# Optimization experiments

Measured on AMD Instinct MI355X. Metric: run time of the kernel, lower is better.

Reference implementation:

```python
import jax, jax.numpy as jnp
import numpy as np

TEMP = 0.05          # args.temp_lp_loss
NUM_CLASSES = 256

def _l2norm(x):
    return x / jnp.linalg.norm(x, axis=-1, keepdims=True)

def setup_inputs() -> dict:
    key = jax.random.key(0)
    k1, k2, k3 = jax.random.split(key, 3)
    B, C, Bs, TOPK = 2048, 2048, 4096, 4
    feats = _l2norm(jax.random.normal(k1, (B, C), jnp.float32))
    feats_s = _l2norm(jax.random.normal(k2, (Bs, TOPK, C), jnp.float32))
    labels = jax.random.randint(k3, (B,), 0, NUM_CLASSES, dtype=jnp.int32)
    # every class 0..255 appears, so each query has >=1 positive support
    labels_s = jnp.arange(Bs * TOPK, dtype=jnp.int32) % NUM_CLASSES
    return {"feats": feats, "feats_s": feats_s, "labels": labels, "labels_s": labels_s}

def reference(feats, feats_s, labels, labels_s):
    Bs, topk, C = feats_s.shape
    fs = feats_s.reshape(Bs * topk, C)                    # [N, C]
    E = jnp.exp(jnp.einsum('bc,nc->bn', feats, fs) / TEMP)  # [B, N]
    is_pos = labels[:, None] == labels_s[None, :]          # [B, N]
    # per-row hardest positive (min over positives of exp-sim)
    pos_min = jnp.min(jnp.where(is_pos, E, jnp.inf), axis=1)   # [B]
    # sum over all negatives of exp-sim
    neg_sum = jnp.sum(jnp.where(is_pos, 0.0, E), axis=1)       # [B]
    loss = -jnp.log(pos_min / (pos_min + neg_sum + 1e-6) + 1e-6)
    return jnp.mean(loss)
```

## Files before the change

kernel.cpp:

```cpp
#include <hip/hip_runtime.h>
#include <hip/hip_bf16.h>
#include <stdint.h>

#define M_TOTAL 2048
#define N_TOTAL 16384
#define K_TOTAL 2048
#define NPARTS  256

#define SCALE_E8M0 0x76767676
#define SCALE_F 512.0f

typedef __attribute__((ext_vector_type(4))) int   int4v;
typedef __attribute__((ext_vector_type(8))) int   int8v;
typedef __attribute__((ext_vector_type(4))) float floatx4;

__global__ void cvt_fp8(const float4* __restrict__ src, uint32_t* __restrict__ dst, int n4) {
    int i = blockIdx.x * blockDim.x + threadIdx.x;
    const int stride = gridDim.x * blockDim.x;
    for (; i < n4; i += stride) {
        float4 v = src[i];
        int p = __builtin_amdgcn_cvt_pk_fp8_f32(v.x * SCALE_F, v.y * SCALE_F, 0, 0);
        p = __builtin_amdgcn_cvt_pk_fp8_f32(v.z * SCALE_F, v.w * SCALE_F, p, 1);
        dst[i] = (uint32_t)p;
    }
}

__device__ __forceinline__ void load16(const void* g, void* l) {
    __builtin_amdgcn_global_load_lds(
        (const __attribute__((address_space(1))) void*)g,
        (__attribute__((address_space(3))) void*)l, 16, 0, 0);
}

__global__ __launch_bounds__(256) void gemm_lp(
        const char* __restrict__ Af8, const char* __restrict__ Bf8,
        const int* __restrict__ labels, const int* __restrict__ labels_s,
        float* __restrict__ pminp, float* __restrict__ psump) {
    __shared__ __align__(16) char lsA[2][128 * 128];
    __shared__ __align__(16) char lsB[2][128 * 128];
    __shared__ int lab_m[128];
    __shared__ int lab_n[128];

    const int t    = threadIdx.x;
    const int lane = t & 63;
    const int wave = t >> 6;
    const int wm   = wave >> 1;
    const int wn   = wave & 1;
    const int m0   = blockIdx.y * 128;
    const int n0   = blockIdx.x * 128;

    if (t < 128) lab_m[t] = labels[m0 + t];
    else         lab_n[t - 128] = labels_s[n0 + t - 128];

    const int rq = t >> 3;
    const int qt = (t & 7) ^ ((t >> 3) & 7);
    const char* aPtr = Af8 + (long)(m0 + rq) * K_TOTAL + qt * 16;
    const char* bPtr = Bf8 + (long)(n0 + rq) * K_TOTAL + qt * 16;
    const int ldsOff = wave * 1024;

    const int quad = lane >> 4;
    const int lcol = lane & 15;
    const int plo = ((2 * quad) ^ (lcol & 7)) << 4;
    const int phi = ((2 * quad + 1) ^ (lcol & 7)) << 4;
    const int aRow = (wm * 64 + lcol) * 128;
    const int bRow = (wn * 64 + lcol) * 128;

    floatx4 acc[4][4];
#pragma unroll
    for (int mi = 0; mi < 4; ++mi)
#pragma unroll
        for (int ni = 0; ni < 4; ++ni)
            acc[mi][ni] = (floatx4){0.f, 0.f, 0.f, 0.f};

#define ISSUE_LOADS(tile, p)                                                  \
    do {                                                                      \
        _Pragma("unroll")                                                     \
        for (int j = 0; j < 4; ++j) {                                         \
            load16(aPtr + (tile) * 128 + j * 32 * K_TOTAL, lsA[p] + ldsOff + j * 4096); \
            load16(bPtr + (tile) * 128 + j * 32 * K_TOTAL, lsB[p] + ldsOff + j * 4096); \
        }                                                                     \
    } while (0)

#define COMPUTE(p)                                                            \
    do {                                                                      \
        int8v bv[4];                                                          \
        _Pragma("unroll")                                                     \
        for (int i = 0; i < 4; ++i) {                                         \
            int4v lo = *(const int4v*)(lsB[p] + bRow + i * 2048 + plo);       \
            int4v hi = *(const int4v*)(lsB[p] + bRow + i * 2048 + phi);       \
            bv[i] = (int8v){lo.x, lo.y, lo.z, lo.w, hi.x, hi.y, hi.z, hi.w};  \
        }                                                                     \
        _Pragma("unroll")                                                     \
        for (int mi = 0; mi < 4; ++mi) {                                      \
            int4v lo = *(const int4v*)(lsA[p] + aRow + mi * 2048 + plo);      \
            int4v hi = *(const int4v*)(lsA[p] + aRow + mi * 2048 + phi);      \
            int8v av = (int8v){lo.x, lo.y, lo.z, lo.w, hi.x, hi.y, hi.z, hi.w}; \
            _Pragma("unroll")                                                 \
            for (int ni = 0; ni < 4; ++ni)                                    \
                acc[mi][ni] = __builtin_amdgcn_mfma_scale_f32_16x16x128_f8f6f4( \
                    av, bv[ni], acc[mi][ni], 0, 0,                            \
                    0, SCALE_E8M0, 0, SCALE_E8M0);                            \
        }                                                                     \
    } while (0)

    ISSUE_LOADS(0, 0);

#pragma unroll 1
    for (int kt2 = 0; kt2 < K_TOTAL / 256; ++kt2) {
        __syncthreads();
        ISSUE_LOADS(1, 1);
        COMPUTE(0);
        __syncthreads();
        if (kt2 < K_TOTAL / 256 - 1)
            ISSUE_LOADS(2, 0);
        COMPUTE(1);
        aPtr += 256;
        bPtr += 256;
    }
#undef ISSUE_LOADS
#undef COMPUTE

    const float scale = 28.853900817779268f;
#pragma unroll
    for (int mi = 0; mi < 4; ++mi) {
#pragma unroll
        for (int r = 0; r < 4; ++r) {
            const int row_local = wm * 64 + mi * 16 + quad * 4 + r;
            const int lab = lab_m[row_local];
            float minv = __builtin_inff();
            float sumv = 0.f;
#pragma unroll
            for (int ni = 0; ni < 4; ++ni) {
                const int col_local = wn * 64 + ni * 16 + lcol;
                const float e = exp2f(acc[mi][ni][r] * scale);
                const bool pos = (lab_n[col_local] == lab);
                minv = pos ? fminf(minv, e) : minv;
                sumv = pos ? sumv : (sumv + e);
            }
#pragma unroll
            for (int off = 1; off < 16; off <<= 1) {
                minv = fminf(minv, __shfl_xor(minv, off, 16));
                sumv += __shfl_xor(sumv, off, 16);
            }
            if (lcol == 0) {
                const long idx = (long)(m0 + row_local) * NPARTS + blockIdx.x * 2 + wn;
                pminp[idx] = minv;
                psump[idx] = sumv;
            }
        }
    }
}

__global__ __launch_bounds__(256) void reduce_rows(
        const float* __restrict__ pminp, const float* __restrict__ psump,
        float* __restrict__ loss) {
    const int row  = blockIdx.x * 4 + (threadIdx.x >> 6);
    const int lane = threadIdx.x & 63;
    float m = __builtin_inff();
    float s = 0.f;
#pragma unroll
    for (int k = 0; k < NPARTS / 64; ++k) {
        const long j = (long)row * NPARTS + lane + k * 64;
        m = fminf(m, pminp[j]);
        s += psump[j];
    }
#pragma unroll
    for (int off = 1; off < 64; off <<= 1) {
        m = fminf(m, __shfl_xor(m, off, 64));
        s += __shfl_xor(s, off, 64);
    }
    if (lane == 0) loss[row] = -logf(m / (m + s + 1e-6f) + 1e-6f);
}

__global__ void final_mean(const float* __restrict__ loss, float* __restrict__ out) {
    float s = 0.f;
    for (int i = threadIdx.x; i < M_TOTAL; i += 256) s += loss[i];
#pragma unroll
    for (int off = 32; off > 0; off >>= 1) s += __shfl_xor(s, off, 64);
    __shared__ float wsum[4];
    if ((threadIdx.x & 63) == 0) wsum[threadIdx.x >> 6] = s;
    __syncthreads();
    if (threadIdx.x == 0)
        out[0] = (wsum[0] + wsum[1] + wsum[2] + wsum[3]) * (1.0f / (float)M_TOTAL);
}

extern "C" void kernel_launch(void* const* d_in, const int* in_sizes, int n_in,
                              void* d_out, int out_size, void* d_ws, size_t ws_size,
                              hipStream_t stream) {
    const float* feats    = (const float*)d_in[0];
    const float* feats_s  = (const float*)d_in[1];
    const int*   labels   = (const int*)d_in[2];
    const int*   labels_s = (const int*)d_in[3];
    float*       out      = (float*)d_out;

    char* ws = (char*)d_ws;
    char*  Af8   = ws;
    char*  Bf8   = ws + 4194304;
    float* pminp = (float*)(ws + 37748736);
    float* psump = (float*)(ws + 39845888);
    float* loss  = (float*)(ws + 41943040);

    cvt_fp8<<<512,  256, 0, stream>>>((const float4*)feats,   (uint32_t*)Af8,
                                      M_TOTAL * K_TOTAL / 4);
    cvt_fp8<<<2048, 256, 0, stream>>>((const float4*)feats_s, (uint32_t*)Bf8,
                                      N_TOTAL * K_TOTAL / 4);

    dim3 grid(N_TOTAL / 128, M_TOTAL / 128);
    gemm_lp<<<grid, 256, 0, stream>>>(Af8, Bf8, labels, labels_s, pminp, psump);

    reduce_rows<<<512, 256, 0, stream>>>(pminp, psump, loss);
    final_mean<<<1, 256, 0, stream>>>(loss, out);
}
```

Before: 307.3 us.

## Merge fp8 conversion launches and switch GEMM to single-buffered 256-wide K tiles

Combines the two fp8 conversion kernels into one launch to save a kernel launch. In the GEMM, replaces the double-buffered 128-wide K tiles with one 256-wide K tile per iteration and a new 16-way XOR swizzle. Each stage now loads, waits on a barrier, then computes two MFMA steps. This halves barriers per K but removes the overlap of loads with compute, so memory latency is exposed.

New measurement: 297.4 us. 3.2% less time.

```diff
diff --git a/kernel.cpp b/kernel.cpp
--- a/kernel.cpp
+++ b/kernel.cpp
@@ -14,9 +14,9 @@
 typedef __attribute__((ext_vector_type(8))) int   int8v;
 typedef __attribute__((ext_vector_type(4))) float floatx4;
 
-__global__ void cvt_fp8(const float4* __restrict__ src, uint32_t* __restrict__ dst, int n4) {
-    int i = blockIdx.x * blockDim.x + threadIdx.x;
-    const int stride = gridDim.x * blockDim.x;
+__device__ __forceinline__ void cvt_loop(const float4* __restrict__ src,
+                                         uint32_t* __restrict__ dst,
+                                         int i, int stride, int n4) {
     for (; i < n4; i += stride) {
         float4 v = src[i];
         int p = __builtin_amdgcn_cvt_pk_fp8_f32(v.x * SCALE_F, v.y * SCALE_F, 0, 0);
@@ -25,6 +25,16 @@
     }
 }
 
+__global__ void cvt_fp8_all(const float4* __restrict__ a, const float4* __restrict__ b,
+                            uint32_t* __restrict__ oa, uint32_t* __restrict__ ob) {
+    if (blockIdx.x < 512)
+        cvt_loop(a, oa, blockIdx.x * 256 + threadIdx.x, 512 * 256,
+                 M_TOTAL * K_TOTAL / 4);
+    else
+        cvt_loop(b, ob, (blockIdx.x - 512) * 256 + threadIdx.x, 2048 * 256,
+                 N_TOTAL * K_TOTAL / 4);
+}
+
 __device__ __forceinline__ void load16(const void* g, void* l) {
     __builtin_amdgcn_global_load_lds(
         (const __attribute__((address_space(1))) void*)g,
@@ -35,8 +45,8 @@
         const char* __restrict__ Af8, const char* __restrict__ Bf8,
         const int* __restrict__ labels, const int* __restrict__ labels_s,
         float* __restrict__ pminp, float* __restrict__ psump) {
-    __shared__ __align__(16) char lsA[2][128 * 128];
-    __shared__ __align__(16) char lsB[2][128 * 128];
+    __shared__ __align__(16) char lsA[128 * 256];
+    __shared__ __align__(16) char lsB[128 * 256];
     __shared__ int lab_m[128];
     __shared__ int lab_n[128];
 
@@ -51,18 +61,20 @@
     if (t < 128) lab_m[t] = labels[m0 + t];
     else         lab_n[t - 128] = labels_s[n0 + t - 128];
 
-    const int rq = t >> 3;
-    const int qt = (t & 7) ^ ((t >> 3) & 7);
+    const int rq = t >> 4;
+    const int qt = (t & 15) ^ (t >> 4);
     const char* aPtr = Af8 + (long)(m0 + rq) * K_TOTAL + qt * 16;
     const char* bPtr = Bf8 + (long)(n0 + rq) * K_TOTAL + qt * 16;
     const int ldsOff = wave * 1024;
 
     const int quad = lane >> 4;
     const int lcol = lane & 15;
-    const int plo = ((2 * quad) ^ (lcol & 7)) << 4;
-    const int phi = ((2 * quad + 1) ^ (lcol & 7)) << 4;
-    const int aRow = (wm * 64 + lcol) * 128;
-    const int bRow = (wn * 64 + lcol) * 128;
+    const int aRow = (wm * 64 + lcol) * 256;
+    const int bRow = (wn * 64 + lcol) * 256;
+    const int lo0 = ((2 * quad)     ^ lcol) << 4;
+    const int hi0 = ((2 * quad + 1) ^ lcol) << 4;
+    const int lo1 = ((8 + 2 * quad)     ^ lcol) << 4;
+    const int hi1 = ((8 + 2 * quad + 1) ^ lcol) << 4;
 
     floatx4 acc[4][4];
 #pragma unroll
@@ -71,28 +83,19 @@
         for (int ni = 0; ni < 4; ++ni)
             acc[mi][ni] = (floatx4){0.f, 0.f, 0.f, 0.f};
 
-#define ISSUE_LOADS(tile, p)                                                  \
-    do {                                                                      \
-        _Pragma("unroll")                                                     \
-        for (int j = 0; j < 4; ++j) {                                         \
-            load16(aPtr + (tile) * 128 + j * 32 * K_TOTAL, lsA[p] + ldsOff + j * 4096); \
-            load16(bPtr + (tile) * 128 + j * 32 * K_TOTAL, lsB[p] + ldsOff + j * 4096); \
-        }                                                                     \
-    } while (0)
-
-#define COMPUTE(p)                                                            \
+#define COMPUTE_STEP(plo, phi)                                                \
     do {                                                                      \
         int8v bv[4];                                                          \
         _Pragma("unroll")                                                     \
         for (int i = 0; i < 4; ++i) {                                         \
-            int4v lo = *(const int4v*)(lsB[p] + bRow + i * 2048 + plo);       \
-            int4v hi = *(const int4v*)(lsB[p] + bRow + i * 2048 + phi);       \
+            int4v lo = *(const int4v*)(lsB + bRow + i * 4096 + (phi ? 0 : 0) + plo); \
+            int4v hi = *(const int4v*)(lsB + bRow + i * 4096 + phi);          \
             bv[i] = (int8v){lo.x, lo.y, lo.z, lo.w, hi.x, hi.y, hi.z, hi.w};  \
         }                                                                     \
         _Pragma("unroll")                                                     \
         for (int mi = 0; mi < 4; ++mi) {                                      \
-            int4v lo = *(const int4v*)(lsA[p] + aRow + mi * 2048 + plo);      \
-            int4v hi = *(const int4v*)(lsA[p] + aRow + mi * 2048 + phi);      \
+            int4v lo = *(const int4v*)(lsA + aRow + mi * 4096 + plo);         \
+            int4v hi = *(const int4v*)(lsA + aRow + mi * 4096 + phi);         \
             int8v av = (int8v){lo.x, lo.y, lo.z, lo.w, hi.x, hi.y, hi.z, hi.w}; \
             _Pragma("unroll")                                                 \
             for (int ni = 0; ni < 4; ++ni)                                    \
@@ -102,22 +105,21 @@
         }                                                                     \
     } while (0)
 
-    ISSUE_LOADS(0, 0);
-
 #pragma unroll 1
-    for (int kt2 = 0; kt2 < K_TOTAL / 256; ++kt2) {
+    for (int kt = 0; kt < K_TOTAL / 256; ++kt) {
         __syncthreads();
-        ISSUE_LOADS(1, 1);
-        COMPUTE(0);
-        __syncthreads();
-        if (kt2 < K_TOTAL / 256 - 1)
-            ISSUE_LOADS(2, 0);
-        COMPUTE(1);
+#pragma unroll
+        for (int j = 0; j < 8; ++j) {
+            load16(aPtr + (long)j * 16 * K_TOTAL, lsA + ldsOff + j * 4096);
+            load16(bPtr + (long)j * 16 * K_TOTAL, lsB + ldsOff + j * 4096);
+        }
         aPtr += 256;
         bPtr += 256;
-    }
-#undef ISSUE_LOADS
-#undef COMPUTE
+        __syncthreads();
+        COMPUTE_STEP(lo0, hi0);
+        COMPUTE_STEP(lo1, hi1);
+    }
+#undef COMPUTE_STEP
 
     const float scale = 28.853900817779268f;
 #pragma unroll
@@ -199,10 +201,8 @@
     float* psump = (float*)(ws + 39845888);
     float* loss  = (float*)(ws + 41943040);
 
-    cvt_fp8<<<512,  256, 0, stream>>>((const float4*)feats,   (uint32_t*)Af8,
-                                      M_TOTAL * K_TOTAL / 4);
-    cvt_fp8<<<2048, 256, 0, stream>>>((const float4*)feats_s, (uint32_t*)Bf8,
-                                      N_TOTAL * K_TOTAL / 4);
+    cvt_fp8_all<<<2560, 256, 0, stream>>>((const float4*)feats, (const float4*)feats_s,
+                                          (uint32_t*)Af8, (uint32_t*)Bf8);
 
     dim3 grid(N_TOTAL / 128, M_TOTAL / 128);
     gemm_lp<<<grid, 256, 0, stream>>>(Af8, Bf8, labels, labels_s, pminp, psump);
```
